# Performance work log

Hardware: AMD Instinct MI355X
Metric: run time of the kernel (lower is better)

The kernel has to match this reference:

```python
import jax, jax.numpy as jnp
import numpy as np

B, S, D, H = 4, 2048, 1024, 16
HD = D // H  # head size = 64

def setup_inputs() -> dict:
    key = jax.random.key(0)
    ks = jax.random.split(key, 9)
    s = 1.0 / np.sqrt(D)
    inp = {"x": jax.random.normal(ks[0], (B, S, D), dtype=jnp.float32)}
    for i, n in enumerate(["q", "k", "v", "o"]):
        inp[f"W{n}"] = jax.random.uniform(ks[1 + 2 * i], (D, D), minval=-s, maxval=s, dtype=jnp.float32)
        inp[f"b{n}"] = jax.random.uniform(ks[2 + 2 * i], (D,), minval=-s, maxval=s, dtype=jnp.float32)
    return inp

def reference(x, Wq, bq, Wk, bk, Wv, bv, Wo, bo):
    b, s, d = x.shape
    # project and split heads: [b, h, s, hd]
    def heads(y):
        return y.reshape(b, s, H, HD).transpose(0, 2, 1, 3)
    q = heads(x @ Wq.T + bq)
    k = heads(x @ Wk.T + bk)
    v = heads(x @ Wv.T + bv)
    scores = jnp.einsum('bhqd,bhkd->bhqk', q, k) / jnp.sqrt(jnp.float32(HD))
    attn = jax.nn.softmax(scores, axis=-1)
    ctx = jnp.einsum('bhqk,bhkd->bhqd', attn, v)
    ctx = ctx.transpose(0, 2, 1, 3).reshape(b, s, d)
    return ctx @ Wo.T + bo
```

## Files before the change

### kernel.cpp

```cpp
#include <hip/hip_runtime.h>
#include <hip/hip_bf16.h>

typedef __bf16 bf16;
typedef __bf16 bf16x8 __attribute__((ext_vector_type(8)));
typedef __bf16 bf16x4 __attribute__((ext_vector_type(4)));
typedef float f32x4 __attribute__((ext_vector_type(4)));
typedef float f32x16 __attribute__((ext_vector_type(16)));
typedef unsigned int u32;
typedef u32 u32x4 __attribute__((ext_vector_type(4)));

#define B_ 4
#define S_ 2048
#define D_ 1024
#define H_ 16
#define HD_ 64
#define LOG2E 1.4426950408889634f

static __device__ __forceinline__ f32x4 mfma16(bf16x8 a, bf16x8 b, f32x4 c) {
  return __builtin_amdgcn_mfma_f32_16x16x32_bf16(a, b, c, 0, 0, 0);
}
static __device__ __forceinline__ f32x16 mfma32(bf16x8 a, bf16x8 b, f32x16 c) {
  return __builtin_amdgcn_mfma_f32_32x32x16_bf16(a, b, c, 0, 0, 0);
}
static __device__ __forceinline__ void gload_lds16(const void* g, void* l) {
  __builtin_amdgcn_global_load_lds(
      (const __attribute__((address_space(1))) void*)g,
      (__attribute__((address_space(3))) void*)l, 16, 0, 0);
}
static __device__ __forceinline__ u32 pack2(float lo, float hi) {
  union { bf16 h[2]; u32 u; } un;
  un.h[0] = (bf16)lo; un.h[1] = (bf16)hi;
  return un.u;
}

__global__ void cvt_kernel(const float* __restrict__ in, bf16* __restrict__ out, int n4) {
  int i = blockIdx.x * blockDim.x + threadIdx.x;
  const int stride = gridDim.x * blockDim.x;
  for (; i < n4; i += stride) {
    float4 v = reinterpret_cast<const float4*>(in)[i];
    bf16x4 o;
    o[0] = (bf16)v.x; o[1] = (bf16)v.y; o[2] = (bf16)v.z; o[3] = (bf16)v.w;
    reinterpret_cast<bf16x4*>(out)[i] = o;
  }
}
__global__ void cvtw_kernel(const float* __restrict__ w0, const float* __restrict__ w1,
                            const float* __restrict__ w2, const float* __restrict__ w3,
                            bf16* __restrict__ o0, bf16* __restrict__ o1,
                            bf16* __restrict__ o2, bf16* __restrict__ o3, int n4) {
  const float* in = blockIdx.y == 0 ? w0 : blockIdx.y == 1 ? w1 : blockIdx.y == 2 ? w2 : w3;
  bf16* out = blockIdx.y == 0 ? o0 : blockIdx.y == 1 ? o1 : blockIdx.y == 2 ? o2 : o3;
  const int i = blockIdx.x * blockDim.x + threadIdx.x;
  float4 v = reinterpret_cast<const float4*>(in)[i];
  bf16x4 o;
  o[0] = (bf16)v.x; o[1] = (bf16)v.y; o[2] = (bf16)v.z; o[3] = (bf16)v.w;
  reinterpret_cast<bf16x4*>(out)[i] = o;
}

template<bool OUT_BF16, bool BIAS_ROW>
__global__ __launch_bounds__(512, 2)
void gemm2(const bf16* __restrict__ A, const bf16* __restrict__ W,
           const float* __restrict__ bias, void* __restrict__ Cout,
           int M, int N, int K, float scale) {
  __shared__ __align__(16) char lds[147456];
  const int tid = threadIdx.x;
  const int wave = tid >> 6;
  const int lane = tid & 63;
  const int g = lane >> 4, r16 = lane & 15;
  const int m0 = blockIdx.y * 256, n0 = blockIdx.x * 128;
  const int wm = (wave >> 1) * 64, wn = (wave & 1) * 64;

  f32x4 acc[4][4] = {};

  const int srow = tid >> 3;
  const int scol = ((tid & 7) ^ (srow & 7)) * 8;
  const int wdst = wave * 1024;
  const int nkt = K >> 6;

  auto stage = [&](int bi, int t) {
    char* buf = lds + bi * 49152;
    const int kb = t << 6;
#pragma unroll
    for (int q = 0; q < 4; ++q)
      gload_lds16(&A[(size_t)(m0 + q * 64 + srow) * K + kb + scol],
                  buf + q * 8192 + wdst);
#pragma unroll
    for (int q = 0; q < 2; ++q)
      gload_lds16(&W[(size_t)(n0 + q * 64 + srow) * K + kb + scol],
                  buf + 32768 + q * 8192 + wdst);
  };

  stage(0, 0);
  stage(1, 1);
  int cur = 0;

  for (int t = 0; t < nkt; ++t) {
    if (t + 1 < nkt) asm volatile("s_waitcnt vmcnt(6)" ::: "memory");
    else             asm volatile("s_waitcnt vmcnt(0)" ::: "memory");
    __builtin_amdgcn_s_barrier();
    int nx2 = cur + 2; if (nx2 >= 3) nx2 -= 3;
    if (t + 2 < nkt) stage(nx2, t + 2);

    const char* bufA = lds + cur * 49152;
    const char* bufB = bufA + 32768;
#pragma unroll
    for (int kk = 0; kk < 2; ++kk) {
      bf16x8 af[4], bfr[4];
#pragma unroll
      for (int i = 0; i < 4; ++i) {
        const int ra = wm + i * 16 + r16;
        af[i]  = *reinterpret_cast<const bf16x8*>(
            bufA + ra * 128 + (((4 * kk + g) ^ (ra & 7)) * 16));
        const int rb = wn + i * 16 + r16;
        bfr[i] = *reinterpret_cast<const bf16x8*>(
            bufB + rb * 128 + (((4 * kk + g) ^ (rb & 7)) * 16));
      }
      __builtin_amdgcn_s_setprio(1);
#pragma unroll
      for (int i = 0; i < 4; ++i)
#pragma unroll
        for (int j = 0; j < 4; ++j)
          acc[i][j] = mfma16(af[i], bfr[j], acc[i][j]);
      __builtin_amdgcn_s_setprio(0);
    }
    cur = (cur + 1 == 3) ? 0 : cur + 1;
  }

#pragma unroll
  for (int i = 0; i < 4; ++i) {
#pragma unroll
    for (int j = 0; j < 4; ++j) {
      const int col = n0 + wn + j * 16 + r16;
      float bcol = BIAS_ROW ? 0.f : bias[col];
#pragma unroll
      for (int r = 0; r < 4; ++r) {
        const int row = m0 + wm + i * 16 + g * 4 + r;
        const float bv = BIAS_ROW ? bias[row] : bcol;
        const float v = (acc[i][j][r] + bv) * scale;
        if (OUT_BF16)
          reinterpret_cast<bf16*>(Cout)[(size_t)row * N + col] = (bf16)v;
        else
          reinterpret_cast<float*>(Cout)[(size_t)row * N + col] = v;
      }
    }
  }
}

__global__ __launch_bounds__(256)
void attn_kernel(const bf16* __restrict__ Q, const bf16* __restrict__ K,
                 const bf16* __restrict__ Vt, bf16* __restrict__ CTX) {
  const unsigned nwg = gridDim.x * gridDim.y;
  const unsigned lid = blockIdx.x + gridDim.x * blockIdx.y;
  const unsigned swzid = (lid & 7) * (nwg >> 3) + (lid >> 3);
  const int bh = (int)(swzid >> 4);
  const int q0 = (int)(swzid & 15) * 128;
  const int h = bh & (H_ - 1), b = bh >> 4;
  const int tid = threadIdx.x, wave = tid >> 6, lane = tid & 63;
  const int l32 = lane & 31, hi = lane >> 5;

  const bf16* Qb  = Q  + ((size_t)b * S_) * D_ + h * HD_;
  const bf16* Kb  = K  + ((size_t)b * S_) * D_ + h * HD_;
  const bf16* Vtb = Vt + (size_t)(h * HD_) * (B_ * S_) + b * S_;

  __shared__ __align__(16) char lds[32768];
  char* const kb0 = lds;
  char* const kb1 = lds + 8192;
  char* const vb0 = lds + 16384;
  char* const vb1 = lds + 24576;

  const int q = q0 + wave * 32 + l32;
  bf16x8 qf[4];
#pragma unroll
  for (int ks = 0; ks < 4; ++ks)
    qf[ks] = *reinterpret_cast<const bf16x8*>(&Qb[(size_t)q * D_ + ks * 16 + hi * 8]);

  bf16x8 onesf;
#pragma unroll
  for (int j = 0; j < 8; ++j) onesf[j] = (bf16)1.0f;

  f32x16 ctx0 = {}, ctx1 = {};
  f32x16 lacc = {};

  const int krow0 = wave * 16 + (lane >> 3);
  const int xs = ((lane & 7) ^ (lane >> 3)) * 8;
  const int stoff = wave * 2048;
  const int swl = (l32 & 7) << 4;
  int coa[4];
#pragma unroll
  for (int ks = 0; ks < 4; ++ks) coa[ks] = (ks * 32 + hi * 16) ^ swl;
  const int rA = l32 * 128, rB = (32 + l32) * 128;

  const bf16* Kst = Kb  + (size_t)krow0 * D_ + xs;
  const bf16* Vst = Vtb + (size_t)krow0 * (B_ * S_) + xs;

  auto stage = [&](char* kd, char* vd) {
    gload_lds16(Kst,                  kd + stoff);
    gload_lds16(Kst + 8 * D_,         kd + stoff + 1024);
    gload_lds16(Vst,                  vd + stoff);
    gload_lds16(Vst + 8 * (B_ * S_),  vd + stoff + 1024);
    Kst += 64 * D_;
    Vst += 64;
  };

  auto compute = [&](const char* bK, const char* bV) {
    f32x16 s0, s1;
    const f32x16 z = {};
    __builtin_amdgcn_s_setprio(1);
    {
      bf16x8 kf0 = *reinterpret_cast<const bf16x8*>(bK + rA + coa[0]);
      bf16x8 kf1 = *reinterpret_cast<const bf16x8*>(bK + rB + coa[0]);
      s0 = mfma32(kf0, qf[0], z);
      s1 = mfma32(kf1, qf[0], z);
    }
#pragma unroll
    for (int ks = 1; ks < 4; ++ks) {
      bf16x8 kf0 = *reinterpret_cast<const bf16x8*>(bK + rA + coa[ks]);
      bf16x8 kf1 = *reinterpret_cast<const bf16x8*>(bK + rB + coa[ks]);
      s0 = mfma32(kf0, qf[ks], s0);
      s1 = mfma32(kf1, qf[ks], s1);
    }
    __builtin_amdgcn_s_setprio(0);
    u32 w0[8], w1[8];
#pragma unroll
    for (int a = 0; a < 4; ++a)
#pragma unroll
      for (int c = 0; c < 2; ++c) {
        w0[2 * a + c] = pack2(__builtin_amdgcn_exp2f(s0[4 * a + 2 * c]),
                              __builtin_amdgcn_exp2f(s0[4 * a + 2 * c + 1]));
        w1[2 * a + c] = pack2(__builtin_amdgcn_exp2f(s1[4 * a + 2 * c]),
                              __builtin_amdgcn_exp2f(s1[4 * a + 2 * c + 1]));
      }
#pragma unroll
    for (int T = 0; T < 2; ++T) {
      const u32* w = T ? w1 : w0;
#pragma unroll
      for (int k1 = 0; k1 < 2; ++k1) {
        auto rAp = __builtin_amdgcn_permlane32_swap((int)w[4 * k1 + 0], (int)w[4 * k1 + 2], false, false);
        auto rBp = __builtin_amdgcn_permlane32_swap((int)w[4 * k1 + 1], (int)w[4 * k1 + 3], false, false);
        u32x4 fw;
        fw[0] = (u32)rAp[0]; fw[1] = (u32)rBp[0]; fw[2] = (u32)rAp[1]; fw[3] = (u32)rBp[1];
        const bf16x8 pa = __builtin_bit_cast(bf16x8, fw);
        const int co = coa[T * 2 + k1];
        bf16x8 vf0 = *reinterpret_cast<const bf16x8*>(bV + rA + co);
        bf16x8 vf1 = *reinterpret_cast<const bf16x8*>(bV + rB + co);
        __builtin_amdgcn_s_setprio(1);
        lacc = mfma32(pa, onesf, lacc);
        ctx0 = mfma32(pa, vf0, ctx0);
        ctx1 = mfma32(pa, vf1, ctx1);
        __builtin_amdgcn_s_setprio(0);
      }
    }
  };

  stage(kb0, vb0);
  __syncthreads();
  for (int tt = 0; tt < 15; ++tt) {
    stage(kb1, vb1);
    compute(kb0, vb0);
    __syncthreads();
    stage(kb0, vb0);
    compute(kb1, vb1);
    __syncthreads();
  }
  stage(kb1, vb1);
  compute(kb0, vb0);
  __syncthreads();
  compute(kb1, vb1);
  __syncthreads();

  char* Cw = lds + wave * 4096;
#pragma unroll
  for (int rg = 0; rg < 16; ++rg) {
    const int ql = (rg & 3) + 8 * (rg >> 2) + 4 * hi;
    const float inv = 1.0f / lacc[rg];
    const int swq = (ql & 7) << 4;
    *reinterpret_cast<bf16*>(Cw + ql * 128 + ((l32 * 2) ^ swq)) = (bf16)(ctx0[rg] * inv);
    *reinterpret_cast<bf16*>(Cw + ql * 128 + ((64 + l32 * 2) ^ swq)) = (bf16)(ctx1[rg] * inv);
  }
  asm volatile("" ::: "memory");
#pragma unroll
  for (int i = 0; i < 4; ++i) {
    const int s = i * 64 + lane;
    const int row = s >> 3, cs = (s & 7) * 16;
    bf16x8 v = *reinterpret_cast<const bf16x8*>(Cw + row * 128 + (cs ^ ((row & 7) << 4)));
    *reinterpret_cast<bf16x8*>(
        &CTX[(size_t)(b * S_ + q0 + wave * 32 + row) * D_ + h * HD_ + cs / 2]) = v;
  }
}

extern "C" void kernel_launch(void* const* d_in, const int* in_sizes, int n_in,
                              void* d_out, int out_size, void* d_ws, size_t ws_size,
                              hipStream_t stream) {
  const float* x  = (const float*)d_in[0];
  const float* Wq = (const float*)d_in[1]; const float* bq = (const float*)d_in[2];
  const float* Wk = (const float*)d_in[3]; const float* bk = (const float*)d_in[4];
  const float* Wv = (const float*)d_in[5]; const float* bv = (const float*)d_in[6];
  const float* Wo = (const float*)d_in[7]; const float* bo = (const float*)d_in[8];

  char* ws = (char*)d_ws;
  const size_t MB = 1048576;
  bf16* xb  = (bf16*)(ws);
  bf16* wqb = (bf16*)(ws + 16 * MB);
  bf16* wkb = (bf16*)(ws + 18 * MB);
  bf16* wvb = (bf16*)(ws + 20 * MB);
  bf16* wob = (bf16*)(ws + 22 * MB);
  bf16* qb  = (bf16*)(ws + 24 * MB);
  bf16* kb  = (bf16*)(ws + 40 * MB);
  bf16* vtb = (bf16*)(ws + 56 * MB);
  bf16* ctx = (bf16*)(ws + 72 * MB);

  cvt_kernel<<<2048, 256, 0, stream>>>(x, xb, 2097152);
  cvtw_kernel<<<dim3(1024, 4), 256, 0, stream>>>(Wq, Wk, Wv, Wo, wqb, wkb, wvb, wob, 262144);

  dim3 gq(1024 / 128, 8192 / 256);
  gemm2<true,  false><<<gq, 512, 0, stream>>>(xb, wqb, bq, qb, 8192, 1024, 1024, 0.125f * LOG2E);
  gemm2<true,  false><<<gq, 512, 0, stream>>>(xb, wkb, bk, kb, 8192, 1024, 1024, 1.0f);
  dim3 gv(8192 / 128, 1024 / 256);
  gemm2<true,  true ><<<gv, 512, 0, stream>>>(wvb, xb, bv, vtb, 1024, 8192, 1024, 1.0f);

  attn_kernel<<<dim3(2048 / 128, B_ * H_), 256, 0, stream>>>(qb, kb, vtb, ctx);

  gemm2<false, false><<<gq, 512, 0, stream>>>(ctx, wob, bo, d_out, 8192, 1024, 1024, 1.0f);
}
```

Baseline: 203.1 us.

## Double attention Q tile per wave and deepen K/V prefetch to four stages

Each wave now handles 64 query rows instead of 32, so every K/V tile loaded into LDS is reused across twice as many queries. The grid shrinks to 512 blocks. The K/V staging goes from a two-buffer scheme with full __syncthreads to a four-buffer ring that waits on vmcnt before each barrier, keeping more global loads in flight. This raises register and LDS use (64KB) and reduces occupancy and block count, which risks latency exposure and poorer load balance across CUs.

```diff
diff --git a/kernel.cpp b/kernel.cpp
--- a/kernel.cpp
+++ b/kernel.cpp
@@ -145,14 +145,17 @@
   }
 }
 
-__global__ __launch_bounds__(256)
+#define VMB(N) do { asm volatile("s_waitcnt vmcnt(" #N ")" ::: "memory"); \
+                    __builtin_amdgcn_s_barrier(); } while (0)
+
+__global__ __launch_bounds__(256, 2)
 void attn_kernel(const bf16* __restrict__ Q, const bf16* __restrict__ K,
                  const bf16* __restrict__ Vt, bf16* __restrict__ CTX) {
   const unsigned nwg = gridDim.x * gridDim.y;
   const unsigned lid = blockIdx.x + gridDim.x * blockIdx.y;
   const unsigned swzid = (lid & 7) * (nwg >> 3) + (lid >> 3);
-  const int bh = (int)(swzid >> 4);
-  const int q0 = (int)(swzid & 15) * 128;
+  const int bh = (int)(swzid >> 3);
+  const int q0 = (int)(swzid & 7) * 256;
   const int h = bh & (H_ - 1), b = bh >> 4;
   const int tid = threadIdx.x, wave = tid >> 6, lane = tid & 63;
   const int l32 = lane & 31, hi = lane >> 5;
@@ -161,24 +164,26 @@
   const bf16* Kb  = K  + ((size_t)b * S_) * D_ + h * HD_;
   const bf16* Vtb = Vt + (size_t)(h * HD_) * (B_ * S_) + b * S_;
 
-  __shared__ __align__(16) char lds[32768];
-  char* const kb0 = lds;
-  char* const kb1 = lds + 8192;
-  char* const vb0 = lds + 16384;
-  char* const vb1 = lds + 24576;
-
-  const int q = q0 + wave * 32 + l32;
-  bf16x8 qf[4];
-#pragma unroll
-  for (int ks = 0; ks < 4; ++ks)
-    qf[ks] = *reinterpret_cast<const bf16x8*>(&Qb[(size_t)q * D_ + ks * 16 + hi * 8]);
+  __shared__ __align__(16) char lds[65536];
+  char* const kb0 = lds;             char* const vb0 = lds + 32768;
+  char* const kb1 = lds + 8192;      char* const vb1 = lds + 40960;
+  char* const kb2 = lds + 16384;     char* const vb2 = lds + 49152;
+  char* const kb3 = lds + 24576;     char* const vb3 = lds + 57344;
+
+  const int qbase = q0 + wave * 64;
+  bf16x8 qf0[4], qf1[4];
+#pragma unroll
+  for (int ks = 0; ks < 4; ++ks) {
+    qf0[ks] = *reinterpret_cast<const bf16x8*>(&Qb[(size_t)(qbase + l32) * D_ + ks * 16 + hi * 8]);
+    qf1[ks] = *reinterpret_cast<const bf16x8*>(&Qb[(size_t)(qbase + 32 + l32) * D_ + ks * 16 + hi * 8]);
+  }
 
   bf16x8 onesf;
 #pragma unroll
   for (int j = 0; j < 8; ++j) onesf[j] = (bf16)1.0f;
 
-  f32x16 ctx0 = {}, ctx1 = {};
-  f32x16 lacc = {};
+  f32x16 ctx00 = {}, ctx01 = {}, ctx10 = {}, ctx11 = {};
+  f32x16 lacc0 = {}, lacc1 = {};
 
   const int krow0 = wave * 16 + (lane >> 3);
   const int xs = ((lane & 7) ^ (lane >> 3)) * 8;
@@ -201,89 +206,121 @@
     Vst += 64;
   };
 
+  auto expack = [&](const f32x16& s, u32* w) {
+#pragma unroll
+    for (int a = 0; a < 4; ++a)
+#pragma unroll
+      for (int c = 0; c < 2; ++c)
+        w[2 * a + c] = pack2(__builtin_amdgcn_exp2f(s[4 * a + 2 * c]),
+                             __builtin_amdgcn_exp2f(s[4 * a + 2 * c + 1]));
+  };
+
   auto compute = [&](const char* bK, const char* bV) {
-    f32x16 s0, s1;
+    bf16x8 kf0[4], kf1[4];
+#pragma unroll
+    for (int ks = 0; ks < 4; ++ks) {
+      kf0[ks] = *reinterpret_cast<const bf16x8*>(bK + rA + coa[ks]);
+      kf1[ks] = *reinterpret_cast<const bf16x8*>(bK + rB + coa[ks]);
+    }
     const f32x16 z = {};
+    f32x16 s00, s01;
     __builtin_amdgcn_s_setprio(1);
-    {
-      bf16x8 kf0 = *reinterpret_cast<const bf16x8*>(bK + rA + coa[0]);
-      bf16x8 kf1 = *reinterpret_cast<const bf16x8*>(bK + rB + coa[0]);
-      s0 = mfma32(kf0, qf[0], z);
-      s1 = mfma32(kf1, qf[0], z);
-    }
+    s00 = mfma32(kf0[0], qf0[0], z);
+    s01 = mfma32(kf1[0], qf0[0], z);
 #pragma unroll
     for (int ks = 1; ks < 4; ++ks) {
-      bf16x8 kf0 = *reinterpret_cast<const bf16x8*>(bK + rA + coa[ks]);
-      bf16x8 kf1 = *reinterpret_cast<const bf16x8*>(bK + rB + coa[ks]);
-      s0 = mfma32(kf0, qf[ks], s0);
-      s1 = mfma32(kf1, qf[ks], s1);
+      s00 = mfma32(kf0[ks], qf0[ks], s00);
+      s01 = mfma32(kf1[ks], qf0[ks], s01);
     }
     __builtin_amdgcn_s_setprio(0);
-    u32 w0[8], w1[8];
-#pragma unroll
-    for (int a = 0; a < 4; ++a)
-#pragma unroll
-      for (int c = 0; c < 2; ++c) {
-        w0[2 * a + c] = pack2(__builtin_amdgcn_exp2f(s0[4 * a + 2 * c]),
-                              __builtin_amdgcn_exp2f(s0[4 * a + 2 * c + 1]));
-        w1[2 * a + c] = pack2(__builtin_amdgcn_exp2f(s1[4 * a + 2 * c]),
-                              __builtin_amdgcn_exp2f(s1[4 * a + 2 * c + 1]));
+    u32 w00[8], w01[8];
+    expack(s00, w00); expack(s01, w01);
+    f32x16 s10, s11;
+    __builtin_amdgcn_s_setprio(1);
+    s10 = mfma32(kf0[0], qf1[0], z);
+    s11 = mfma32(kf1[0], qf1[0], z);
+#pragma unroll
+    for (int ks = 1; ks < 4; ++ks) {
+      s10 = mfma32(kf0[ks], qf1[ks], s10);
+      s11 = mfma32(kf1[ks], qf1[ks], s11);
+    }
+    __builtin_amdgcn_s_setprio(0);
+    u32 w10[8], w11[8];
+    expack(s10, w10); expack(s11, w11);
+    bf16x8 vf0[4], vf1[4];
+#pragma unroll
+    for (int ksp = 0; ksp < 4; ++ksp) {
+      vf0[ksp] = *reinterpret_cast<const bf16x8*>(bV + rA + coa[ksp]);
+      vf1[ksp] = *reinterpret_cast<const bf16x8*>(bV + rB + coa[ksp]);
+    }
+#pragma unroll
+    for (int m = 0; m < 2; ++m) {
+      const u32* wlo = m ? w10 : w00;
+      const u32* whi = m ? w11 : w01;
+      f32x16& la = m ? lacc1 : lacc0;
+      f32x16& c0 = m ? ctx10 : ctx00;
+      f32x16& c1 = m ? ctx11 : ctx01;
+#pragma unroll
+      for (int T = 0; T < 2; ++T) {
+        const u32* w = T ? whi : wlo;
+#pragma unroll
+        for (int k1 = 0; k1 < 2; ++k1) {
+          auto rAp = __builtin_amdgcn_permlane32_swap((int)w[4 * k1 + 0], (int)w[4 * k1 + 2], false, false);
+          auto rBp = __builtin_amdgcn_permlane32_swap((int)w[4 * k1 + 1], (int)w[4 * k1 + 3], false, false);
+          u32x4 fw;
+          fw[0] = (u32)rAp[0]; fw[1] = (u32)rBp[0]; fw[2] = (u32)rAp[1]; fw[3] = (u32)rBp[1];
+          const bf16x8 pa = __builtin_bit_cast(bf16x8, fw);
+          const int ksp = 2 * T + k1;
+          __builtin_amdgcn_s_setprio(1);
+          la = mfma32(pa, onesf, la);
+          c0 = mfma32(pa, vf0[ksp], c0);
+          c1 = mfma32(pa, vf1[ksp], c1);
+          __builtin_amdgcn_s_setprio(0);
+        }
       }
-#pragma unroll
-    for (int T = 0; T < 2; ++T) {
-      const u32* w = T ? w1 : w0;
-#pragma unroll
-      for (int k1 = 0; k1 < 2; ++k1) {
-        auto rAp = __builtin_amdgcn_permlane32_swap((int)w[4 * k1 + 0], (int)w[4 * k1 + 2], false, false);
-        auto rBp = __builtin_amdgcn_permlane32_swap((int)w[4 * k1 + 1], (int)w[4 * k1 + 3], false, false);
-        u32x4 fw;
-        fw[0] = (u32)rAp[0]; fw[1] = (u32)rBp[0]; fw[2] = (u32)rAp[1]; fw[3] = (u32)rBp[1];
-        const bf16x8 pa = __builtin_bit_cast(bf16x8, fw);
-        const int co = coa[T * 2 + k1];
-        bf16x8 vf0 = *reinterpret_cast<const bf16x8*>(bV + rA + co);
-        bf16x8 vf1 = *reinterpret_cast<const bf16x8*>(bV + rB + co);
-        __builtin_amdgcn_s_setprio(1);
-        lacc = mfma32(pa, onesf, lacc);
-        ctx0 = mfma32(pa, vf0, ctx0);
-        ctx1 = mfma32(pa, vf1, ctx1);
-        __builtin_amdgcn_s_setprio(0);
-      }
     }
   };
 
   stage(kb0, vb0);
+  stage(kb1, vb1);
+  stage(kb2, vb2);
+
+  for (int u = 0; u < 7; ++u) {
+    VMB(8); stage(kb3, vb3); compute(kb0, vb0);
+    VMB(8); stage(kb0, vb0); compute(kb1, vb1);
+    VMB(8); stage(kb1, vb1); compute(kb2, vb2);
+    VMB(8); stage(kb2, vb2); compute(kb3, vb3);
+  }
+  VMB(8); stage(kb3, vb3); compute(kb0, vb0);
+  VMB(8); compute(kb1, vb1);
+  VMB(4); compute(kb2, vb2);
+  VMB(0); compute(kb3, vb3);
   __syncthreads();
-  for (int tt = 0; tt < 15; ++tt) {
-    stage(kb1, vb1);
-    compute(kb0, vb0);
-    __syncthreads();
-    stage(kb0, vb0);
-    compute(kb1, vb1);
-    __syncthreads();
-  }
-  stage(kb1, vb1);
-  compute(kb0, vb0);
-  __syncthreads();
-  compute(kb1, vb1);
-  __syncthreads();
-
-  char* Cw = lds + wave * 4096;
+
+  char* Cw = lds + wave * 8192;
 #pragma unroll
   for (int rg = 0; rg < 16; ++rg) {
     const int ql = (rg & 3) + 8 * (rg >> 2) + 4 * hi;
-    const float inv = 1.0f / lacc[rg];
     const int swq = (ql & 7) << 4;
-    *reinterpret_cast<bf16*>(Cw + ql * 128 + ((l32 * 2) ^ swq)) = (bf16)(ctx0[rg] * inv);
-    *reinterpret_cast<bf16*>(Cw + ql * 128 + ((64 + l32 * 2) ^ swq)) = (bf16)(ctx1[rg] * inv);
+    {
+      const float inv = 1.0f / lacc0[rg];
+      *reinterpret_cast<bf16*>(Cw + ql * 128 + ((l32 * 2) ^ swq)) = (bf16)(ctx00[rg] * inv);
+      *reinterpret_cast<bf16*>(Cw + ql * 128 + ((64 + l32 * 2) ^ swq)) = (bf16)(ctx01[rg] * inv);
+    }
+    {
+      const float inv = 1.0f / lacc1[rg];
+      *reinterpret_cast<bf16*>(Cw + (32 + ql) * 128 + ((l32 * 2) ^ swq)) = (bf16)(ctx10[rg] * inv);
+      *reinterpret_cast<bf16*>(Cw + (32 + ql) * 128 + ((64 + l32 * 2) ^ swq)) = (bf16)(ctx11[rg] * inv);
+    }
   }
   asm volatile("" ::: "memory");
 #pragma unroll
-  for (int i = 0; i < 4; ++i) {
+  for (int i = 0; i < 8; ++i) {
     const int s = i * 64 + lane;
     const int row = s >> 3, cs = (s & 7) * 16;
     bf16x8 v = *reinterpret_cast<const bf16x8*>(Cw + row * 128 + (cs ^ ((row & 7) << 4)));
     *reinterpret_cast<bf16x8*>(
-        &CTX[(size_t)(b * S_ + q0 + wave * 32 + row) * D_ + h * HD_ + cs / 2]) = v;
+        &CTX[(size_t)(b * S_ + q0 + wave * 64 + row) * D_ + h * HD_ + cs / 2]) = v;
   }
 }
 
@@ -317,7 +354,7 @@
   dim3 gv(8192 / 128, 1024 / 256);
   gemm2<true,  true ><<<gv, 512, 0, stream>>>(wvb, xb, bv, vtb, 1024, 8192, 1024, 1.0f);
 
-  attn_kernel<<<dim3(2048 / 128, B_ * H_), 256, 0, stream>>>(qb, kb, vtb, ctx);
+  attn_kernel<<<dim3(8, 64), 256, 0, stream>>>(qb, kb, vtb, ctx);
 
   gemm2<false, false><<<gq, 512, 0, stream>>>(ctx, wob, bo, d_out, 8192, 1024, 1024, 1.0f);
 }
```

New measurement: 193.1 us. 5.0% less time.
